# Performance work log

Measured on AMD Instinct MI355X. Metric: run time of the kernel, lower is better.

The kernel has to match this reference:

```python
import jax, jax.numpy as jnp
import numpy as np

DIM = 2048
NUM_HEADS = 16
HEAD_DIM = DIM // NUM_HEADS
WINDOW_SIZE = 3072
SCALE = HEAD_DIM ** (-0.5)
NEG_INF = -1e9


def setup_inputs() -> dict:
    key = jax.random.key(0)
    ks = jax.random.split(key, 6)
    B, N = 2, 2048
    x = jax.random.normal(ks[0], (B, N, DIM), dtype=jnp.float32)
    w_init = 0.02
    Wq = jax.random.normal(ks[1], (DIM, DIM), dtype=jnp.float32) * w_init
    Wk = jax.random.normal(ks[2], (DIM, DIM), dtype=jnp.float32) * w_init
    Wv = jax.random.normal(ks[3], (DIM, DIM), dtype=jnp.float32) * w_init
    Wo = jax.random.normal(ks[4], (DIM, DIM), dtype=jnp.float32) * w_init
    zeros = jnp.zeros((DIM,), dtype=jnp.float32)
    return {"x": x, "Wq": Wq, "bq": zeros, "Wk": Wk, "bk": zeros,
            "Wv": Wv, "bv": zeros, "Wo": Wo, "bo": zeros}


def _window_mask(q_len: int, kv_len: int) -> jnp.ndarray:
    # Faithful to SlidingWindowAttention._window_mask with causal=True:
    # row i allows j in [max(0, kv_len - window_size + i), i]; mask=True means blocked.
    i = jnp.arange(q_len)[:, None]
    j = jnp.arange(kv_len)[None, :]
    start = jnp.maximum(0, kv_len - WINDOW_SIZE + i)
    allowed = (j >= start) & (j <= i)  # second term is the causal triu complement
    return ~allowed  # [q_len, kv_len] bool, True = masked


def reference(x, Wq, bq, Wk, bk, Wv, bv, Wo, bo):
    B, N, C = x.shape
    H, D = NUM_HEADS, HEAD_DIM
    # torch nn.Linear: y = x @ W.T + b
    q = (x @ Wq.T + bq).reshape(B, N, H, D).transpose(0, 2, 1, 3)  # [B,H,N,D]
    k = (x @ Wk.T + bk).reshape(B, N, H, D).transpose(0, 2, 1, 3)
    v = (x @ Wv.T + bv).reshape(B, N, H, D).transpose(0, 2, 1, 3)

    scores = jnp.einsum('bhqd,bhkd->bhqk', q, k) * SCALE  # [B,H,N,N]
    mask = _window_mask(N, N)  # [N,N]
    scores = jnp.where(mask[None, None], NEG_INF, scores)
    attn = jax.nn.softmax(scores, axis=-1)
    out = jnp.einsum('bhqk,bhkd->bhqd', attn, v)  # [B,H,N,D]
    out = out.transpose(0, 2, 1, 3).reshape(B, N, C)
    return out @ Wo.T + bo
```

## Files before the change

### kernel.cpp

```cpp
#include <hip/hip_runtime.h>
#include <cstdint>

#define DIMC 2048
#define NSEQ 2048
#define BATCH 2
#define NH 16
#define HD 128
#define MROWS 4096
#define NQKV 6144
#define QSCALE 0.08838834764831845f

typedef float f32x4 __attribute__((ext_vector_type(4)));
typedef __bf16 bf16x8 __attribute__((ext_vector_type(8)));
typedef __bf16 bf16x4 __attribute__((ext_vector_type(4)));

__device__ __forceinline__ f32x4 mfma16(bf16x8 a, bf16x8 b, f32x4 c) {
  return __builtin_amdgcn_mfma_f32_16x16x32_bf16(a, b, c, 0, 0, 0);
}

typedef __attribute__((address_space(1))) void gvoid;
typedef __attribute__((address_space(3))) void ldsvoid;

__device__ __forceinline__ void async16(void* lds, const void* g) {
  __builtin_amdgcn_global_load_lds((gvoid*)(uintptr_t)g, (ldsvoid*)(uintptr_t)lds, 16, 0, 0);
}

#define BAR() asm volatile("s_barrier" ::: "memory")
#define VMCNT0() asm volatile("s_waitcnt vmcnt(0)" ::: "memory")

__global__ __launch_bounds__(256) void cast_all(const float* __restrict__ x,
                                                const float* __restrict__ Wq,
                                                const float* __restrict__ Wk,
                                                const float* __restrict__ Wv,
                                                const float* __restrict__ Wo,
                                                __bf16* __restrict__ xb,
                                                __bf16* __restrict__ Wqkvb,
                                                __bf16* __restrict__ Wob) {
  const int i = (blockIdx.x * 256 + threadIdx.x) * 4;
  const int WN = DIMC * DIMC;
  const float* s;
  __bf16* d;
  if (i < MROWS * DIMC) { s = x + i; d = xb + i; }
  else {
    const int j = i - MROWS * DIMC;
    const int m = j / WN, r = j - m * WN;
    s = ((m == 0) ? Wq : (m == 1) ? Wk : (m == 2) ? Wv : Wo) + r;
    d = ((m == 3) ? Wob : Wqkvb + (size_t)m * WN) + r;
  }
  const float4 v = *(const float4*)s;
  bf16x4 o = {(__bf16)v.x, (__bf16)v.y, (__bf16)v.z, (__bf16)v.w};
  *(bf16x4*)d = o;
}

template <int EPI>
__global__ __launch_bounds__(256) void gemm_bt(
    const __bf16* __restrict__ A, const __bf16* __restrict__ Bm,
    __bf16* __restrict__ Qb, __bf16* __restrict__ Kb, __bf16* __restrict__ Vtb,
    const float* __restrict__ bias0, const float* __restrict__ bias1,
    const float* __restrict__ bias2, float* __restrict__ outp) {
  __shared__ __bf16 Al[128 * 64];
  __shared__ __bf16 Bl[128 * 64];
  const int tid = threadIdx.x;
  const int w = tid >> 6, l = tid & 63;
  const int a = l & 15, g = l >> 4;
  const int mbase = blockIdx.y * 128, nbase = blockIdx.x * 128;
  const int wr = w >> 1, wc = w & 1;

  f32x4 acc[4][4] = {};

  const int rlane = l >> 3;
  const int chunk = ((l & 7) ^ rlane) * 16;
  const char* Ag = (const char*)A + (size_t)(mbase + rlane) * (DIMC * 2) + chunk;
  const char* Bg = (const char*)Bm + (size_t)(nbase + rlane) * (DIMC * 2) + chunk;

  for (int kt = 0; kt < DIMC / 64; ++kt) {
    const size_t ko = (size_t)kt * 128;
#pragma unroll
    for (int j = 0; j < 4; ++j) {
      const int o = w * 4 + j;
      const size_t roff = (size_t)o * 8 * (DIMC * 2) + ko;
      async16((char*)Al + o * 1024, Ag + roff);
      async16((char*)Bl + o * 1024, Bg + roff);
    }
    __syncthreads();
#pragma unroll
    for (int ks = 0; ks < 2; ++ks) {
      bf16x8 af[4], bf_[4];
      const int cxe = ((ks * 4 + g) ^ (a & 7)) * 16;
#pragma unroll
      for (int m = 0; m < 4; ++m)
        af[m] = *(const bf16x8*)((const char*)Al + (wr * 64 + m * 16 + a) * 128 + cxe);
#pragma unroll
      for (int n = 0; n < 4; ++n)
        bf_[n] = *(const bf16x8*)((const char*)Bl + (wc * 64 + n * 16 + a) * 128 + cxe);
#pragma unroll
      for (int m = 0; m < 4; ++m)
#pragma unroll
        for (int n = 0; n < 4; ++n) acc[m][n] = mfma16(af[m], bf_[n], acc[m][n]);
    }
    __syncthreads();
  }

  if constexpr (EPI == 0) {
    const int seg = nbase >> 11;
    const int cin = (nbase & 2047) + wc * 64;
    const float* bias = (seg == 0) ? bias0 : ((seg == 1) ? bias1 : bias2);
    const float scl = (seg == 0) ? QSCALE : 1.0f;
#pragma unroll
    for (int n = 0; n < 4; ++n) {
      const int c = cin + n * 16 + a;
      const float bb = bias[c];
      const int h = c >> 7, d = c & 127;
#pragma unroll
      for (int m = 0; m < 4; ++m) {
        const int mr = mbase + wr * 64 + m * 16 + g * 4;
        const int b_ = mr >> 11, sq = mr & 2047;
        f32x4 v = acc[m][n];
        if (seg == 2) {
          __bf16* dst = Vtb + ((size_t)(b_ * NH + h) * HD + d) * NSEQ + sq;
          bf16x4 pk = {(__bf16)(v[0] + bb), (__bf16)(v[1] + bb),
                       (__bf16)(v[2] + bb), (__bf16)(v[3] + bb)};
          *(bf16x4*)dst = pk;
        } else {
          __bf16* dst = ((seg == 0) ? Qb : Kb) +
                        ((size_t)(b_ * NH + h) * NSEQ + sq) * HD + d;
#pragma unroll
          for (int j = 0; j < 4; ++j) dst[(size_t)j * HD] = (__bf16)((v[j] + bb) * scl);
        }
      }
    }
  } else {
#pragma unroll
    for (int n = 0; n < 4; ++n) {
      const int c = nbase + wc * 64 + n * 16 + a;
      const float bb = bias0[c];
#pragma unroll
      for (int m = 0; m < 4; ++m) {
        const int mr = mbase + wr * 64 + m * 16 + g * 4;
        float* dst = outp + (size_t)mr * DIMC + c;
        f32x4 v = acc[m][n];
#pragma unroll
        for (int j = 0; j < 4; ++j) dst[(size_t)j * DIMC] = v[j] + bb;
      }
    }
  }
}

__global__ __launch_bounds__(512) void attn_swa6(const __bf16* __restrict__ Qb,
                                                 const __bf16* __restrict__ Kb,
                                                 const __bf16* __restrict__ Vtb,
                                                 __bf16* __restrict__ Ob) {
  extern __shared__ __align__(16) char AL[];
  const int tid = threadIdx.x;
  const int w = tid >> 6, l = tid & 63;
  const int a = l & 15, g = l >> 4;
  const int id = blockIdx.x;
  const int bh = (id & 7) + ((id >> 6) << 3);
  const int qbase = ((id >> 3) & 7) * 256;
  const __bf16* Qg = Qb + (size_t)bh * NSEQ * HD;
  const char* Kg = (const char*)(Kb + (size_t)bh * NSEQ * HD);
  const char* Vg = (const char*)(Vtb + (size_t)bh * HD * NSEQ);

  bf16x8 qf[2][4];
#pragma unroll
  for (int qi = 0; qi < 2; ++qi)
#pragma unroll
    for (int s = 0; s < 4; ++s)
      qf[qi][s] = *(const bf16x8*)(Qg + (size_t)(qbase + w * 32 + qi * 16 + a) * HD + s * 32 + g * 8);

  float mrow[2] = {-1e38f, -1e38f}, lrow[2] = {0.f, 0.f};
  f32x4 o[2][8] = {};

  const int ktlo = (qbase >= 1024) ? ((qbase - 1024) >> 6) : 0;
  const int kthi = (qbase + 255) >> 6;

  auto stage = [&](int b, int kt) {
    const int kb2 = kt * 64;
    char* Kl = AL + b * 32768;
    char* Vl = AL + b * 32768 + 16384;
#pragma unroll
    for (int j = 0; j < 2; ++j) {
      const int row = j * 32 + (tid >> 4);
      const int ch = (tid & 15) ^ ((tid >> 4) & 7);
      async16(Kl + j * 8192 + w * 1024, Kg + (size_t)(kb2 + row) * 256 + ch * 16);
    }
#pragma unroll
    for (int j = 0; j < 2; ++j) {
      const int row = j * 64 + (tid >> 3);
      const int ch = (tid & 7) ^ ((tid >> 3) & 7);
      async16(Vl + j * 8192 + w * 1024,
              Vg + (size_t)row * (NSEQ * 2) + (size_t)kb2 * 2 + ch * 16);
    }
  };

  stage(0, ktlo);
  VMCNT0(); BAR();
  int buf = 0;
  char* Pw = AL + 65536 + w * 4096;

  for (int kt = ktlo; kt <= kthi; ++kt) {
    if (kt < kthi) stage(buf ^ 1, kt + 1);
    const char* Kl = AL + buf * 32768;
    const char* Vl = AL + buf * 32768 + 16384;
    const int kb2 = kt * 64;
    const bool full = (kb2 >= qbase + 255 - 1024) && (kb2 + 63 <= qbase);

    f32x4 s4[2][4];
#pragma unroll
    for (int t = 0; t < 4; ++t) {
      bf16x8 kf[4];
#pragma unroll
      for (int ds = 0; ds < 4; ++ds)
        kf[ds] = *(const bf16x8*)(Kl + (t * 16 + a) * 256 + (((ds * 4 + g) ^ (a & 7)) * 16));
      __builtin_amdgcn_s_setprio(1);
#pragma unroll
      for (int qi = 0; qi < 2; ++qi) {
        f32x4 sc = {};
#pragma unroll
        for (int ds = 0; ds < 4; ++ds) sc = mfma16(kf[ds], qf[qi][ds], sc);
        s4[qi][t] = sc;
      }
      __builtin_amdgcn_s_setprio(0);
    }

    if (!full) {
#pragma unroll
      for (int qi = 0; qi < 2; ++qi) {
        const int q = qbase + w * 32 + qi * 16 + a;
#pragma unroll
        for (int t = 0; t < 4; ++t)
#pragma unroll
          for (int i = 0; i < 4; ++i) {
            const int kv = kb2 + t * 16 + g * 4 + i;
            if (kv > q || kv + 1024 < q) s4[qi][t][i] = -1e30f;
          }
      }
    }

#pragma unroll
    for (int qi = 0; qi < 2; ++qi) {
      float pm = s4[qi][0][0];
#pragma unroll
      for (int t = 0; t < 4; ++t)
#pragma unroll
        for (int i = 0; i < 4; ++i)
          if (t || i) pm = fmaxf(pm, s4[qi][t][i]);
      pm = fmaxf(pm, __shfl_xor(pm, 16));
      pm = fmaxf(pm, __shfl_xor(pm, 32));
      if (!__all(pm - mrow[qi] <= 8.f)) {
        const float nm = fmaxf(mrow[qi], pm);
        const float corr = __expf(mrow[qi] - nm);
        mrow[qi] = nm;
        lrow[qi] *= corr;
#pragma unroll
        for (int n = 0; n < 8; ++n)
#pragma unroll
          for (int i = 0; i < 4; ++i) o[qi][n][i] *= corr;
      }
      float rs = 0.f;
#pragma unroll
      for (int t = 0; t < 4; ++t)
#pragma unroll
        for (int i = 0; i < 4; ++i) {
          const float p = __expf(s4[qi][t][i] - mrow[qi]);
          s4[qi][t][i] = p;
          rs += p;
        }
      rs += __shfl_xor(rs, 16);
      rs += __shfl_xor(rs, 32);
      lrow[qi] += rs;
      const int prow = qi * 16 + a;
#pragma unroll
      for (int t = 0; t < 4; ++t) {
        bf16x4 pk = {(__bf16)s4[qi][t][0], (__bf16)s4[qi][t][1],
                     (__bf16)s4[qi][t][2], (__bf16)s4[qi][t][3]};
        const int byte = (prow * 128 + (t * 16 + g * 4) * 2) ^ ((a & 7) << 4);
        *(bf16x4*)(Pw + byte) = pk;
      }
    }

#pragma unroll
    for (int ks = 0; ks < 2; ++ks) {
      bf16x8 pa[2];
#pragma unroll
      for (int qi = 0; qi < 2; ++qi)
        pa[qi] = *(const bf16x8*)(Pw + (((qi * 16 + a) * 128 + ks * 64 + g * 16) ^ ((a & 7) << 4)));
#pragma unroll
      for (int n = 0; n < 8; ++n) {
        bf16x8 va = *(const bf16x8*)(Vl + (n * 16 + a) * 128 + (((ks * 4 + g) ^ (a & 7)) * 16));
        __builtin_amdgcn_s_setprio(1);
#pragma unroll
        for (int qi = 0; qi < 2; ++qi) o[qi][n] = mfma16(va, pa[qi], o[qi][n]);
        __builtin_amdgcn_s_setprio(0);
      }
    }

    VMCNT0(); BAR();
    buf ^= 1;
  }

  const int b_ = bh >> 4, h = bh & 15;
#pragma unroll
  for (int qi = 0; qi < 2; ++qi) {
    const int q = qbase + w * 32 + qi * 16 + a;
    const float inv = 1.f / lrow[qi];
    __bf16* Og = Ob + (size_t)(b_ * NSEQ + q) * DIMC + h * HD + g * 4;
#pragma unroll
    for (int n = 0; n < 8; ++n) {
      bf16x4 pk = {(__bf16)(o[qi][n][0] * inv), (__bf16)(o[qi][n][1] * inv),
                   (__bf16)(o[qi][n][2] * inv), (__bf16)(o[qi][n][3] * inv)};
      *(bf16x4*)(Og + (size_t)n * 16) = pk;
    }
  }
}

extern "C" void kernel_launch(void* const* d_in, const int* in_sizes, int n_in,
                              void* d_out, int out_size, void* d_ws, size_t ws_size,
                              hipStream_t stream) {
  const float* x = (const float*)d_in[0];
  const float* Wq = (const float*)d_in[1];
  const float* bq = (const float*)d_in[2];
  const float* Wk = (const float*)d_in[3];
  const float* bk = (const float*)d_in[4];
  const float* Wv = (const float*)d_in[5];
  const float* bv = (const float*)d_in[6];
  const float* Wo = (const float*)d_in[7];
  const float* bo = (const float*)d_in[8];
  float* out = (float*)d_out;

  char* ws = (char*)d_ws;
  __bf16* xb    = (__bf16*)(ws + 0);
  __bf16* Wqkvb = (__bf16*)(ws + 16777216);
  __bf16* Wob   = (__bf16*)(ws + 41943040);
  __bf16* Qb    = (__bf16*)(ws + 50331648);
  __bf16* Kb    = (__bf16*)(ws + 67108864);
  __bf16* Vtb   = (__bf16*)(ws + 83886080);
  __bf16* Ob    = xb;

  (void)hipFuncSetAttribute((const void*)attn_swa6,
                            hipFuncAttributeMaxDynamicSharedMemorySize, 98304);

  cast_all<<<dim3((MROWS * DIMC + 4 * DIMC * DIMC) / 1024), 256, 0, stream>>>(
      x, Wq, Wk, Wv, Wo, xb, Wqkvb, Wob);

  gemm_bt<0><<<dim3(NQKV / 128, MROWS / 128), 256, 0, stream>>>(
      xb, Wqkvb, Qb, Kb, Vtb, bq, bk, bv, nullptr);

  attn_swa6<<<dim3(256), 512, 98304, stream>>>(Qb, Kb, Vtb, Ob);

  gemm_bt<1><<<dim3(DIMC / 128, MROWS / 128), 256, 0, stream>>>(
      Ob, Wob, nullptr, nullptr, nullptr, bo, nullptr, nullptr, out);
}
```

Baseline: 243.8 us.

## Triple-buffer K/V tiles in sliding-window attention with prefetch distance two

Replaces the double-buffered K/V staging in the attention kernel with a three-slot ring that keeps two tiles in flight. Each iteration waits on partial vmcnt and a single barrier before issuing the next prefetch, instead of a full vmcnt(0) plus barrier at the end of every iteration. The aim is to hide global-to-LDS load latency behind the MFMA work. In exchange, LDS use grows to 128 KB per block, and correctness now depends on the hand-counted outstanding-load number.

After: 244.5 us. About the same (+0.3%).

```diff
diff --git a/kernel.cpp b/kernel.cpp
--- a/kernel.cpp
+++ b/kernel.cpp
@@ -26,7 +26,7 @@
 }
 
 #define BAR() asm volatile("s_barrier" ::: "memory")
-#define VMCNT0() asm volatile("s_waitcnt vmcnt(0)" ::: "memory")
+#define VMCNT(n) asm volatile("s_waitcnt vmcnt(" #n ")" ::: "memory")
 
 __global__ __launch_bounds__(256) void cast_all(const float* __restrict__ x,
                                                 const float* __restrict__ Wq,
@@ -146,7 +146,7 @@
   }
 }
 
-__global__ __launch_bounds__(512) void attn_swa6(const __bf16* __restrict__ Qb,
+__global__ __launch_bounds__(512) void attn_swa7(const __bf16* __restrict__ Qb,
                                                  const __bf16* __restrict__ Kb,
                                                  const __bf16* __restrict__ Vtb,
                                                  __bf16* __restrict__ Ob) {
@@ -174,10 +174,10 @@
   const int ktlo = (qbase >= 1024) ? ((qbase - 1024) >> 6) : 0;
   const int kthi = (qbase + 255) >> 6;
 
-  auto stage = [&](int b, int kt) {
+  auto stage = [&](int slot, int kt) {
     const int kb2 = kt * 64;
-    char* Kl = AL + b * 32768;
-    char* Vl = AL + b * 32768 + 16384;
+    char* Kl = AL + slot * 32768;
+    char* Vl = AL + slot * 32768 + 16384;
 #pragma unroll
     for (int j = 0; j < 2; ++j) {
       const int row = j * 32 + (tid >> 4);
@@ -194,14 +194,19 @@
   };
 
   stage(0, ktlo);
-  VMCNT0(); BAR();
-  int buf = 0;
-  char* Pw = AL + 65536 + w * 4096;
+  if (ktlo + 1 <= kthi) stage(1, ktlo + 1);
+  int s = 0;
+  char* Pw = AL + 98304 + w * 4096;
 
   for (int kt = ktlo; kt <= kthi; ++kt) {
-    if (kt < kthi) stage(buf ^ 1, kt + 1);
-    const char* Kl = AL + buf * 32768;
-    const char* Vl = AL + buf * 32768 + 16384;
+    if (kt < kthi) { VMCNT(4); } else { VMCNT(0); }
+    BAR();
+    if (kt + 2 <= kthi) {
+      int s2 = s + 2; if (s2 >= 3) s2 -= 3;
+      stage(s2, kt + 2);
+    }
+    const char* Kl = AL + s * 32768;
+    const char* Vl = AL + s * 32768 + 16384;
     const int kb2 = kt * 64;
     const bool full = (kb2 >= qbase + 255 - 1024) && (kb2 + 63 <= qbase);
 
@@ -295,8 +300,7 @@
       }
     }
 
-    VMCNT0(); BAR();
-    buf ^= 1;
+    s = (s == 2) ? 0 : s + 1;
   }
 
   const int b_ = bh >> 4, h = bh & 15;
@@ -337,8 +341,8 @@
   __bf16* Vtb   = (__bf16*)(ws + 83886080);
   __bf16* Ob    = xb;
 
-  (void)hipFuncSetAttribute((const void*)attn_swa6,
-                            hipFuncAttributeMaxDynamicSharedMemorySize, 98304);
+  (void)hipFuncSetAttribute((const void*)attn_swa7,
+                            hipFuncAttributeMaxDynamicSharedMemorySize, 131072);
 
   cast_all<<<dim3((MROWS * DIMC + 4 * DIMC * DIMC) / 1024), 256, 0, stream>>>(
       x, Wq, Wk, Wv, Wo, xb, Wqkvb, Wob);
@@ -346,7 +350,7 @@
   gemm_bt<0><<<dim3(NQKV / 128, MROWS / 128), 256, 0, stream>>>(
       xb, Wqkvb, Qb, Kb, Vtb, bq, bk, bv, nullptr);
 
-  attn_swa6<<<dim3(256), 512, 98304, stream>>>(Qb, Kb, Vtb, Ob);
+  attn_swa7<<<dim3(256), 512, 131072, stream>>>(Qb, Kb, Vtb, Ob);
 
   gemm_bt<1><<<dim3(DIMC / 128, MROWS / 128), 256, 0, stream>>>(
       Ob, Wob, nullptr, nullptr, nullptr, bo, nullptr, nullptr, out);
```
